# Optimization experiments

Measured on AMD Instinct MI355X. Metric: run time of the kernel, lower is better.

Reference implementation:

```python
import jax, jax.numpy as jnp
import numpy as np

B, T, C, H = 8, 2048, 1024, 64

def setup_inputs() -> dict:
    key = jax.random.key(0)
    k1, k2, k3, k4 = jax.random.split(key, 4)
    x = jax.random.normal(k1, (B, T, C), dtype=jnp.float32)
    sw = 1.0 / np.sqrt(C)  # Linear-like init scale
    Wq = jax.random.normal(k2, (C, H), dtype=jnp.float32) * sw
    Wk = jax.random.normal(k3, (C, H), dtype=jnp.float32) * sw
    Wv = jax.random.normal(k4, (C, H), dtype=jnp.float32) * sw
    return {"x": x, "Wq": Wq, "Wk": Wk, "Wv": Wv}

def reference(x, Wq, Wk, Wv):
    # Single-head causal self-attention (eval mode: dropout is identity).
    # Quantized GEMMs (QLinear / qmatmul) are represented by exact fp32 math.
    Bx, Tx, Cx = x.shape
    q = jnp.einsum('btc,ch->bth', x, Wq)          # [B,T,H]
    k = jnp.einsum('btc,ch->bth', x, Wk)          # [B,T,H]
    v = jnp.einsum('btc,ch->bth', x, Wv)          # [B,T,H]
    scale = k.shape[-1] ** -0.5
    wei = jnp.einsum('bth,bsh->bts', q, k) * scale  # [B,T,T]
    causal = jnp.tril(jnp.ones((Tx, Tx), dtype=bool))
    wei = jnp.where(causal, wei, -jnp.inf)
    wei = jax.nn.softmax(wei, axis=-1)
    out = jnp.einsum('bts,bsh->bth', wei, v)      # [B,T,H]
    return out
```

## Files before the change

kernel.cpp:

```cpp
#include <hip/hip_runtime.h>
#include <math.h>

#define Bz 8
#define Tz 2048
#define Cz 1024
#define Hz 64
#define BT (Bz*Tz)

typedef __attribute__((ext_vector_type(8))) short bf16x8;
typedef __attribute__((ext_vector_type(4))) float f32x4;
typedef __attribute__((ext_vector_type(4))) unsigned short us4;

#define PSTRIDE 4160

__device__ __forceinline__ unsigned short f2bf(float f) {
    union { float f; unsigned u; } v; v.f = f;
    unsigned r = v.u + 0x7fffu + ((v.u >> 16) & 1u);
    return (unsigned short)(r >> 16);
}

__device__ __forceinline__ bf16x8 pack8(const float* s) {
    bf16x8 r;
#pragma unroll
    for (int j = 0; j < 8; j++) r[j] = (short)f2bf(s[j]);
    return r;
}

__device__ __forceinline__ unsigned cvt_pk_bf16(float lo, float hi) {
    unsigned r;
    asm volatile("v_cvt_pk_bf16_f32 %0, %1, %2" : "=v"(r) : "v"(lo), "v"(hi));
    return r;
}

__device__ __forceinline__ bf16x8 cvt8(float4 a, float4 b) {
    union { unsigned u[4]; bf16x8 v; } r;
    r.u[0] = cvt_pk_bf16(a.x, a.y);
    r.u[1] = cvt_pk_bf16(a.z, a.w);
    r.u[2] = cvt_pk_bf16(b.x, b.y);
    r.u[3] = cvt_pk_bf16(b.z, b.w);
    return r.v;
}

__device__ __forceinline__ void gload16(const void* g, void* l) {
    __builtin_amdgcn_global_load_lds(
        (const __attribute__((address_space(1))) void*)g,
        (__attribute__((address_space(3))) void*)l, 16, 0, 0);
}

__global__ __launch_bounds__(256)
void wprep_kernel(const float* __restrict__ Wq, const float* __restrict__ Wk,
                  const float* __restrict__ Wv, unsigned short* __restrict__ Wti)
{
    __shared__ float T[64][65];
    const int mat = blockIdx.x >> 4;
    const int kt  = blockIdx.x & 15;
    const int k0  = kt * 64;
    const float* W = (mat == 0) ? Wq : (mat == 1) ? Wk : Wv;
    const int t  = threadIdx.x;
    const int rr = t >> 2;
    const int c4 = (t & 3) * 16;
#pragma unroll
    for (int j = 0; j < 4; j++) {
        float4 w4 = *(const float4*)&W[(size_t)(k0 + rr) * Hz + c4 + j * 4];
        T[c4 + j*4 + 0][rr] = w4.x;
        T[c4 + j*4 + 1][rr] = w4.y;
        T[c4 + j*4 + 2][rr] = w4.z;
        T[c4 + j*4 + 3][rr] = w4.w;
    }
    __syncthreads();
    const int nn  = t >> 2;
    const int sl0 = (t & 3) * 2;
    const int n   = mat * 64 + nn;
    float tmp[16];
#pragma unroll
    for (int j = 0; j < 16; j++) tmp[j] = T[nn][sl0 * 8 + j];
    unsigned short* base = &Wti[(size_t)kt * 12288 + n * 64];
    *(bf16x8*)&base[((sl0    ) ^ (n & 7)) * 8] = pack8(tmp);
    *(bf16x8*)&base[((sl0 + 1) ^ (n & 7)) * 8] = pack8(tmp + 8);
}

__global__ __launch_bounds__(256, 4)
void qkv_mfma_kernel(const float* __restrict__ x, const unsigned short* __restrict__ Wti,
                     unsigned short* __restrict__ qg, unsigned short* __restrict__ kg,
                     unsigned short* __restrict__ vT)
{
    __shared__ __align__(16) float          xsF[2][64 * 64];
    __shared__ __align__(16) unsigned short ws [2][96 * 64];

    const int t    = threadIdx.x;
    const int bid  = blockIdx.x;
    const int u    = bid >> 3;
    const int cb   = u & 1;
    const int M0   = (((u >> 1) * 8) + (bid & 7)) * 64;
    const int ln   = t & 15;
    const int g    = (t & 63) >> 4;
    const int g4   = g * 4;
    const int w    = t >> 6;
    const int lane = t & 63;
    const float SCq = 0.18033688011112042f;

    f32x4 acc[6];
#pragma unroll
    for (int i = 0; i < 6; i++) acc[i] = (f32x4){0.f, 0.f, 0.f, 0.f};

    auto issue = [&](int buf, int kt) {
        const int k0 = kt * 64;
#pragma unroll
        for (int j = 0; j < 4; j++) {
            const int r  = w * 16 + j * 4 + (lane >> 4);
            const int sl = (lane & 15) ^ (r & 7);
            gload16(&x[(size_t)(M0 + r) * Cz + k0 + sl * 4],
                    &xsF[buf][(w * 16 + j * 4) * 64]);
        }
#pragma unroll
        for (int j = 0; j < 3; j++) {
            const int jj = w * 3 + j;
            gload16(&Wti[(size_t)kt * 12288 + (size_t)(cb * 96 + jj * 8) * 64 + lane * 8],
                    &ws[buf][jj * 512]);
        }
    };

    issue(0, 0); issue(1, 1);
    asm volatile("s_waitcnt vmcnt(7)" ::: "memory");
    __builtin_amdgcn_sched_barrier(0);
    __builtin_amdgcn_s_barrier();

    for (int kt = 0; kt < 16; ++kt) {
        const int bufR = kt & 1;
        bf16x8 af[2];
        const int row = w * 16 + ln;
#pragma unroll
        for (int kc = 0; kc < 2; kc++) {
            const int s0 = kc * 8 + g * 2;
            float4 fa = *(const float4*)&xsF[bufR][row * 64 + ((s0    ) ^ (row & 7)) * 4];
            float4 fb = *(const float4*)&xsF[bufR][row * 64 + ((s0 + 1) ^ (row & 7)) * 4];
            af[kc] = cvt8(fa, fb);
        }
        __builtin_amdgcn_s_setprio(1);
#pragma unroll
        for (int ct = 0; ct < 6; ct++) {
            const int nn = ct * 16 + ln;
#pragma unroll
            for (int kc = 0; kc < 2; kc++) {
                bf16x8 bf = *(const bf16x8*)&ws[bufR][nn * 64 + ((kc*4 + g) ^ (nn & 7)) * 8];
                acc[ct] = __builtin_amdgcn_mfma_f32_16x16x32_bf16(af[kc], bf, acc[ct], 0, 0, 0);
            }
        }
        __builtin_amdgcn_s_setprio(0);

        if (kt == 15) break;

        __builtin_amdgcn_sched_barrier(0);
        __builtin_amdgcn_s_barrier();

        if (kt + 2 < 16) {
            issue(bufR, kt + 2);
            asm volatile("s_waitcnt vmcnt(7)" ::: "memory");
        } else {
            asm volatile("s_waitcnt vmcnt(0)" ::: "memory");
        }
        __builtin_amdgcn_sched_barrier(0);
        __builtin_amdgcn_s_barrier();
    }

#pragma unroll
    for (int ct = 0; ct < 6; ct++) {
        const int col0 = cb * 96 + ct * 16;
        const int mat  = col0 >> 6;
        const int cl   = (col0 & 63) + ln;
        const int m0   = M0 + w * 16 + g4;
        if (mat == 0) {
#pragma unroll
            for (int i = 0; i < 4; i++)
                qg[(size_t)(m0 + i) * Hz + cl] = f2bf(acc[ct][i] * SCq);
        } else if (mat == 1) {
#pragma unroll
            for (int i = 0; i < 4; i++)
                kg[(size_t)(m0 + i) * Hz + cl] = f2bf(acc[ct][i]);
        } else {
            const int b = m0 >> 11, tt = m0 & 2047;
            us4 pk;
#pragma unroll
            for (int i = 0; i < 4; i++) pk[i] = f2bf(acc[ct][i]);
            *(us4*)&vT[((size_t)b * Hz + cl) * Tz + tt] = pk;
        }
    }
}

template<int S>
__global__ __launch_bounds__(256, 4)
void attn_mfma_kernel(const unsigned short* __restrict__ qg,
                      const unsigned short* __restrict__ kg,
                      const unsigned short* __restrict__ vT,
                      float* __restrict__ pbase)
{
    __shared__ __align__(16) unsigned short Ks [2][64 * 64];
    __shared__ __align__(16) unsigned short Vts[2][64 * 64];
    __shared__ __align__(16) unsigned short Ps [4 * 16 * 64];

    const int bid = blockIdx.x;
    const int b   = bid & 7;
    const int r0  = bid >> 3;
    const int c   = r0 % S;
    const int qt  = 31 - (r0 / S);
    if (c > qt) return;
    const int q0  = qt * 64;

    const int t  = threadIdx.x;
    const int ln = t & 15;
    const int g  = (t & 63) >> 4;
    const int g4 = g * 4;
    const int w  = t >> 6;
    const int l6 = t & 63;

    const unsigned short* qb = qg + (size_t)b * Tz * Hz;
    const unsigned short* kb = kg + (size_t)b * Tz * Hz;
    const unsigned short* vb = vT + (size_t)b * Hz * Tz;

    const int rl  = l6 >> 3;
    const int swz = ((l6 & 7) ^ rl) * 8;
    auto issue_tile = [&](int buf, int s0) {
#pragma unroll
        for (int qq = 0; qq < 2; qq++) {
            const int row = w*16 + qq*8 + rl;
            gload16(&kb[(size_t)(s0 + row) * Hz + swz],
                    &Ks[buf][(w*16 + qq*8) * 64]);
            gload16(&vb[(size_t)row * Tz + s0 + swz],
                    &Vts[buf][(w*16 + qq*8) * 64]);
        }
    };

    issue_tile(0, c * 64);

    bf16x8 qf[2];
    {
        const int qrow = q0 + w*16 + ln;
        qf[0] = *(const bf16x8*)&qb[(size_t)qrow * Hz + g*8];
        qf[1] = *(const bf16x8*)&qb[(size_t)qrow * Hz + 32 + g*8];
    }

    f32x4 accO[4];
#pragma unroll
    for (int i = 0; i < 4; i++) accO[i] = (f32x4){0.f, 0.f, 0.f, 0.f};
    float lrow = 0.f;
    unsigned short* Pw = &Ps[w * 1024];
    const int pwbase = ln*64 + (g & 1) * 4;
    const int pslotx = (g >> 1);

    __syncthreads();
    int cur = 0;

    for (int s = c; s <= qt; s += S) {
        if (s + S <= qt) issue_tile(cur ^ 1, (s + S) * 64);

        const unsigned short* Kc = &Ks[cur][0];
        const unsigned short* Vc = &Vts[cur][0];

        f32x4 accS[4];
        __builtin_amdgcn_s_setprio(1);
#pragma unroll
        for (int t4 = 0; t4 < 4; t4++) {
            accS[t4] = (f32x4){0.f, 0.f, 0.f, 0.f};
#pragma unroll
            for (int kc = 0; kc < 2; kc++) {
                const int n = t4*16 + ln;
                bf16x8 kf = *(const bf16x8*)&Kc[n*64 + ((kc*4 + g) ^ (n & 7)) * 8];
                accS[t4] = __builtin_amdgcn_mfma_f32_16x16x32_bf16(kf, qf[kc], accS[t4], 0, 0, 0);
            }
        }
        __builtin_amdgcn_s_setprio(0);

        const bool diag = (s == qt);
#pragma unroll
        for (int t4 = 0; t4 < 4; t4++) {
            float pv[4];
#pragma unroll
            for (int i = 0; i < 4; i++) {
                float sv = accS[t4][i];
                if (diag && (t4*16 + g4 + i > w*16 + ln)) sv = -1e30f;
                const float p = exp2f(sv);
                lrow += p;
                pv[i] = p;
            }
            uint2 pk2;
            pk2.x = cvt_pk_bf16(pv[0], pv[1]);
            pk2.y = cvt_pk_bf16(pv[2], pv[3]);
            *(uint2*)&Pw[pwbase + ((t4*2 + pslotx) ^ (ln & 7)) * 8] = pk2;
        }

        __builtin_amdgcn_s_setprio(1);
#pragma unroll
        for (int kc = 0; kc < 2; kc++) {
            bf16x8 pa = *(const bf16x8*)&Pw[ln*64 + ((kc*4 + g) ^ (ln & 7)) * 8];
#pragma unroll
            for (int ht = 0; ht < 4; ht++) {
                const int vr2 = ht*16 + ln;
                bf16x8 vf = *(const bf16x8*)&Vc[vr2*64 + ((kc*4 + g) ^ (vr2 & 7)) * 8];
                accO[ht] = __builtin_amdgcn_mfma_f32_16x16x32_bf16(pa, vf, accO[ht], 0, 0, 0);
            }
        }
        __builtin_amdgcn_s_setprio(0);

        __syncthreads();
        cur ^= 1;
    }

    lrow += __shfl_xor(lrow, 16);
    lrow += __shfl_xor(lrow, 32);

    float* Op = pbase + (size_t)((b * 32 + qt) * S + c) * PSTRIDE;
#pragma unroll
    for (int ht = 0; ht < 4; ht++)
#pragma unroll
        for (int i = 0; i < 4; i++)
            Op[(size_t)(w*16 + g4 + i) * 64 + ht*16 + ln] = accO[ht][i];
    if (g == 0)
        Op[4096 + w*16 + ln] = lrow;
}

template<int S>
__global__ __launch_bounds__(256)
void combine_kernel(const float* __restrict__ pbase, float* __restrict__ out)
{
    const int bid = blockIdx.x;
    const int b   = bid & 7;
    const int qt  = 31 - (bid >> 3);
    const int t   = threadIdx.x;
    const int r   = t >> 2;
    const int cg  = t & 3;

    const int nch = (qt + 1 < S) ? (qt + 1) : S;
    const float* P0 = pbase + (size_t)(b * 32 + qt) * S * PSTRIDE;

    float denom = 0.f;
    float4 o[4];
#pragma unroll
    for (int j = 0; j < 4; j++) o[j] = make_float4(0.f, 0.f, 0.f, 0.f);
    for (int cc = 0; cc < nch; cc++) {
        const float* Pc = P0 + (size_t)cc * PSTRIDE;
        denom += Pc[4096 + r];
#pragma unroll
        for (int j = 0; j < 4; j++) {
            float4 v4 = *(const float4*)&Pc[(size_t)r * 64 + cg * 16 + j * 4];
            o[j].x += v4.x; o[j].y += v4.y; o[j].z += v4.z; o[j].w += v4.w;
        }
    }
    const float inv = 1.f / denom;
    float* ob = out + ((size_t)b * Tz + qt * 64 + r) * Hz + cg * 16;
#pragma unroll
    for (int j = 0; j < 4; j++)
        *(float4*)&ob[j * 4] = make_float4(o[j].x * inv, o[j].y * inv,
                                           o[j].z * inv, o[j].w * inv);
}

extern "C" void kernel_launch(void* const* d_in, const int* in_sizes, int n_in,
                              void* d_out, int out_size, void* d_ws, size_t ws_size,
                              hipStream_t stream) {
    const float* x  = (const float*)d_in[0];
    const float* Wq = (const float*)d_in[1];
    const float* Wk = (const float*)d_in[2];
    const float* Wv = (const float*)d_in[3];

    unsigned short* Wti = (unsigned short*)d_ws;
    unsigned short* qg  = Wti + 196608;
    unsigned short* kg  = qg + (size_t)BT * Hz;
    unsigned short* vT  = kg + (size_t)BT * Hz;
    const size_t baseShorts = 196608 + 3 * (size_t)BT * Hz;
    float* pbase = (float*)((char*)d_ws + baseShorts * 2);
    float* out = (float*)d_out;

    wprep_kernel<<<48, 256, 0, stream>>>(Wq, Wk, Wv, Wti);
    qkv_mfma_kernel<<<512, 256, 0, stream>>>(x, Wti, qg, kg, vT);

    const size_t base = baseShorts * 2;
    const size_t per  = (size_t)8 * 32 * PSTRIDE * 4;
    if (ws_size >= base + 4 * per) {
        attn_mfma_kernel<4><<<8 * 32 * 4, 256, 0, stream>>>(qg, kg, vT, pbase);
        combine_kernel<4><<<256, 256, 0, stream>>>(pbase, out);
    } else {
        attn_mfma_kernel<1><<<8 * 32 * 1, 256, 0, stream>>>(qg, kg, vT, pbase);
        combine_kernel<1><<<256, 256, 0, stream>>>(pbase, out);
    }
}
```

Measured before the change: 47.88 us.

## Process two query tiles per attention block and store partials in bf16

Each attention block now handles 128 query rows (two 64-row halves) and shares each loaded K/V tile between both halves. This halves K/V global and LDS traffic per query and the number of blocks. Split-K partial outputs are written as bf16 instead of fp32, which cuts partial-buffer traffic for the combine kernel at some precision cost. The block count drops to 512 and per-thread register use rises, which may lower occupancy.

Result: slower. 51.85 us (+8.3%).

```diff
diff --git a/kernel.cpp b/kernel.cpp
--- a/kernel.cpp
+++ b/kernel.cpp
@@ -11,7 +11,7 @@
 typedef __attribute__((ext_vector_type(4))) float f32x4;
 typedef __attribute__((ext_vector_type(4))) unsigned short us4;
 
-#define PSTRIDE 4160
+#define PBYTES 16896
 
 __device__ __forceinline__ unsigned short f2bf(float f) {
     union { float f; unsigned u; } v; v.f = f;
@@ -152,7 +152,6 @@
 
         __builtin_amdgcn_sched_barrier(0);
         __builtin_amdgcn_s_barrier();
-
         if (kt + 2 < 16) {
             issue(bufR, kt + 2);
             asm volatile("s_waitcnt vmcnt(7)" ::: "memory");
@@ -192,7 +191,7 @@
 void attn_mfma_kernel(const unsigned short* __restrict__ qg,
                       const unsigned short* __restrict__ kg,
                       const unsigned short* __restrict__ vT,
-                      float* __restrict__ pbase)
+                      char* __restrict__ pbase)
 {
     __shared__ __align__(16) unsigned short Ks [2][64 * 64];
     __shared__ __align__(16) unsigned short Vts[2][64 * 64];
@@ -200,11 +199,12 @@
 
     const int bid = blockIdx.x;
     const int b   = bid & 7;
-    const int r0  = bid >> 3;
-    const int c   = r0 % S;
-    const int qt  = 31 - (r0 / S);
-    if (c > qt) return;
-    const int q0  = qt * 64;
+    const int idx = bid >> 3;
+    const int c   = idx % S;
+    const int qt2 = 15 - (idx / S);
+    const int smax = 2 * qt2 + 1;
+    if (c > smax) return;
+    const int q0  = qt2 * 128;
 
     const int t  = threadIdx.x;
     const int ln = t & 15;
@@ -232,17 +232,23 @@
 
     issue_tile(0, c * 64);
 
-    bf16x8 qf[2];
+    bf16x8 qf0[2], qf1[2];
     {
-        const int qrow = q0 + w*16 + ln;
-        qf[0] = *(const bf16x8*)&qb[(size_t)qrow * Hz + g*8];
-        qf[1] = *(const bf16x8*)&qb[(size_t)qrow * Hz + 32 + g*8];
-    }
-
-    f32x4 accO[4];
-#pragma unroll
-    for (int i = 0; i < 4; i++) accO[i] = (f32x4){0.f, 0.f, 0.f, 0.f};
-    float lrow = 0.f;
+        const int qr0 = q0 + w*16 + ln;
+        qf0[0] = *(const bf16x8*)&qb[(size_t)qr0 * Hz + g*8];
+        qf0[1] = *(const bf16x8*)&qb[(size_t)qr0 * Hz + 32 + g*8];
+        const int qr1 = q0 + 64 + w*16 + ln;
+        qf1[0] = *(const bf16x8*)&qb[(size_t)qr1 * Hz + g*8];
+        qf1[1] = *(const bf16x8*)&qb[(size_t)qr1 * Hz + 32 + g*8];
+    }
+
+    f32x4 accO0[4], accO1[4];
+#pragma unroll
+    for (int i = 0; i < 4; i++) {
+        accO0[i] = (f32x4){0.f, 0.f, 0.f, 0.f};
+        accO1[i] = (f32x4){0.f, 0.f, 0.f, 0.f};
+    }
+    float lrow0 = 0.f, lrow1 = 0.f;
     unsigned short* Pw = &Ps[w * 1024];
     const int pwbase = ln*64 + (g & 1) * 4;
     const int pslotx = (g >> 1);
@@ -250,107 +256,123 @@
     __syncthreads();
     int cur = 0;
 
-    for (int s = c; s <= qt; s += S) {
-        if (s + S <= qt) issue_tile(cur ^ 1, (s + S) * 64);
+#define DO_HALF(QF, ACCO, LROW, DIAG)                                          \
+    {                                                                          \
+        f32x4 accS[4];                                                         \
+        __builtin_amdgcn_s_setprio(1);                                         \
+        _Pragma("unroll")                                                      \
+        for (int t4 = 0; t4 < 4; t4++) {                                       \
+            accS[t4] = (f32x4){0.f, 0.f, 0.f, 0.f};                            \
+            _Pragma("unroll")                                                  \
+            for (int kc = 0; kc < 2; kc++) {                                   \
+                const int n = t4*16 + ln;                                      \
+                bf16x8 kf = *(const bf16x8*)&Kc[n*64 + ((kc*4 + g) ^ (n & 7)) * 8]; \
+                accS[t4] = __builtin_amdgcn_mfma_f32_16x16x32_bf16(kf, QF[kc], accS[t4], 0, 0, 0); \
+            }                                                                  \
+        }                                                                      \
+        __builtin_amdgcn_s_setprio(0);                                         \
+        _Pragma("unroll")                                                      \
+        for (int t4 = 0; t4 < 4; t4++) {                                       \
+            float pv[4];                                                       \
+            _Pragma("unroll")                                                  \
+            for (int i = 0; i < 4; i++) {                                      \
+                float sv = accS[t4][i];                                        \
+                if ((DIAG) && (t4*16 + g4 + i > w*16 + ln)) sv = -1e30f;       \
+                const float p = exp2f(sv);                                     \
+                LROW += p;                                                     \
+                pv[i] = p;                                                     \
+            }                                                                  \
+            uint2 pk2;                                                         \
+            pk2.x = cvt_pk_bf16(pv[0], pv[1]);                                 \
+            pk2.y = cvt_pk_bf16(pv[2], pv[3]);                                 \
+            *(uint2*)&Pw[pwbase + ((t4*2 + pslotx) ^ (ln & 7)) * 8] = pk2;     \
+        }                                                                      \
+        __builtin_amdgcn_s_setprio(1);                                         \
+        _Pragma("unroll")                                                      \
+        for (int kc = 0; kc < 2; kc++) {                                       \
+            bf16x8 pa = *(const bf16x8*)&Pw[ln*64 + ((kc*4 + g) ^ (ln & 7)) * 8]; \
+            _Pragma("unroll")                                                  \
+            for (int ht = 0; ht < 4; ht++) {                                   \
+                const int vr2 = ht*16 + ln;                                    \
+                bf16x8 vf = *(const bf16x8*)&Vc[vr2*64 + ((kc*4 + g) ^ (vr2 & 7)) * 8]; \
+                ACCO[ht] = __builtin_amdgcn_mfma_f32_16x16x32_bf16(pa, vf, ACCO[ht], 0, 0, 0); \
+            }                                                                  \
+        }                                                                      \
+        __builtin_amdgcn_s_setprio(0);                                         \
+    }
+
+    for (int s = c; s <= smax; s += S) {
+        if (s + S <= smax) issue_tile(cur ^ 1, (s + S) * 64);
 
         const unsigned short* Kc = &Ks[cur][0];
         const unsigned short* Vc = &Vts[cur][0];
 
-        f32x4 accS[4];
-        __builtin_amdgcn_s_setprio(1);
-#pragma unroll
-        for (int t4 = 0; t4 < 4; t4++) {
-            accS[t4] = (f32x4){0.f, 0.f, 0.f, 0.f};
-#pragma unroll
-            for (int kc = 0; kc < 2; kc++) {
-                const int n = t4*16 + ln;
-                bf16x8 kf = *(const bf16x8*)&Kc[n*64 + ((kc*4 + g) ^ (n & 7)) * 8];
-                accS[t4] = __builtin_amdgcn_mfma_f32_16x16x32_bf16(kf, qf[kc], accS[t4], 0, 0, 0);
-            }
-        }
-        __builtin_amdgcn_s_setprio(0);
-
-        const bool diag = (s == qt);
-#pragma unroll
-        for (int t4 = 0; t4 < 4; t4++) {
-            float pv[4];
-#pragma unroll
-            for (int i = 0; i < 4; i++) {
-                float sv = accS[t4][i];
-                if (diag && (t4*16 + g4 + i > w*16 + ln)) sv = -1e30f;
-                const float p = exp2f(sv);
-                lrow += p;
-                pv[i] = p;
-            }
-            uint2 pk2;
-            pk2.x = cvt_pk_bf16(pv[0], pv[1]);
-            pk2.y = cvt_pk_bf16(pv[2], pv[3]);
-            *(uint2*)&Pw[pwbase + ((t4*2 + pslotx) ^ (ln & 7)) * 8] = pk2;
-        }
-
-        __builtin_amdgcn_s_setprio(1);
-#pragma unroll
-        for (int kc = 0; kc < 2; kc++) {
-            bf16x8 pa = *(const bf16x8*)&Pw[ln*64 + ((kc*4 + g) ^ (ln & 7)) * 8];
-#pragma unroll
-            for (int ht = 0; ht < 4; ht++) {
-                const int vr2 = ht*16 + ln;
-                bf16x8 vf = *(const bf16x8*)&Vc[vr2*64 + ((kc*4 + g) ^ (vr2 & 7)) * 8];
-                accO[ht] = __builtin_amdgcn_mfma_f32_16x16x32_bf16(pa, vf, accO[ht], 0, 0, 0);
-            }
-        }
-        __builtin_amdgcn_s_setprio(0);
+        if (s != smax) DO_HALF(qf0, accO0, lrow0, (s == smax - 1));
+        DO_HALF(qf1, accO1, lrow1, (s == smax));
 
         __syncthreads();
         cur ^= 1;
     }
-
-    lrow += __shfl_xor(lrow, 16);
-    lrow += __shfl_xor(lrow, 32);
-
-    float* Op = pbase + (size_t)((b * 32 + qt) * S + c) * PSTRIDE;
+#undef DO_HALF
+
+    lrow0 += __shfl_xor(lrow0, 16); lrow0 += __shfl_xor(lrow0, 32);
+    lrow1 += __shfl_xor(lrow1, 16); lrow1 += __shfl_xor(lrow1, 32);
+
+    char* Op = pbase + (size_t)((b * 16 + qt2) * S + c) * PBYTES;
+    unsigned short* Ob = (unsigned short*)Op;
+    float* Lp = (float*)(Op + 16384);
 #pragma unroll
     for (int ht = 0; ht < 4; ht++)
 #pragma unroll
-        for (int i = 0; i < 4; i++)
-            Op[(size_t)(w*16 + g4 + i) * 64 + ht*16 + ln] = accO[ht][i];
-    if (g == 0)
-        Op[4096 + w*16 + ln] = lrow;
+        for (int i = 0; i < 4; i++) {
+            Ob[(size_t)(w*16 + g4 + i) * 64 + ht*16 + ln]        = f2bf(accO0[ht][i]);
+            Ob[(size_t)(64 + w*16 + g4 + i) * 64 + ht*16 + ln]   = f2bf(accO1[ht][i]);
+        }
+    if (g == 0) {
+        Lp[w*16 + ln]      = lrow0;
+        Lp[64 + w*16 + ln] = lrow1;
+    }
 }
 
 template<int S>
 __global__ __launch_bounds__(256)
-void combine_kernel(const float* __restrict__ pbase, float* __restrict__ out)
+void combine_kernel(const char* __restrict__ pbase, float* __restrict__ out)
 {
     const int bid = blockIdx.x;
     const int b   = bid & 7;
-    const int qt  = 31 - (bid >> 3);
+    const int qt2 = bid >> 3;
     const int t   = threadIdx.x;
-    const int r   = t >> 2;
-    const int cg  = t & 3;
-
-    const int nch = (qt + 1 < S) ? (qt + 1) : S;
-    const float* P0 = pbase + (size_t)(b * 32 + qt) * S * PSTRIDE;
+    const int r   = t >> 1;
+    const int cg  = (t & 1) * 32;
+
+    const int nch = (2*qt2 + 2 < S) ? (2*qt2 + 2) : S;
+    const char* P0 = pbase + (size_t)((b * 16 + qt2) * S) * PBYTES;
 
     float denom = 0.f;
-    float4 o[4];
-#pragma unroll
-    for (int j = 0; j < 4; j++) o[j] = make_float4(0.f, 0.f, 0.f, 0.f);
+    float o[32];
+#pragma unroll
+    for (int j = 0; j < 32; j++) o[j] = 0.f;
     for (int cc = 0; cc < nch; cc++) {
-        const float* Pc = P0 + (size_t)cc * PSTRIDE;
-        denom += Pc[4096 + r];
-#pragma unroll
-        for (int j = 0; j < 4; j++) {
-            float4 v4 = *(const float4*)&Pc[(size_t)r * 64 + cg * 16 + j * 4];
-            o[j].x += v4.x; o[j].y += v4.y; o[j].z += v4.z; o[j].w += v4.w;
+        const char* Pc = P0 + (size_t)cc * PBYTES;
+        const unsigned short* Ob = (const unsigned short*)Pc;
+        denom += ((const float*)(Pc + 16384))[r];
+#pragma unroll
+        for (int j = 0; j < 8; j++) {
+            us4 v = *(const us4*)&Ob[(size_t)r * 64 + cg + j * 4];
+#pragma unroll
+            for (int e = 0; e < 4; e++) {
+                union { unsigned u; float f; } cv;
+                cv.u = ((unsigned)v[e]) << 16;
+                o[j*4 + e] += cv.f;
+            }
         }
     }
     const float inv = 1.f / denom;
-    float* ob = out + ((size_t)b * Tz + qt * 64 + r) * Hz + cg * 16;
-#pragma unroll
-    for (int j = 0; j < 4; j++)
-        *(float4*)&ob[j * 4] = make_float4(o[j].x * inv, o[j].y * inv,
-                                           o[j].z * inv, o[j].w * inv);
+    float* ob = out + ((size_t)b * Tz + qt2 * 128 + r) * Hz + cg;
+#pragma unroll
+    for (int j = 0; j < 8; j++)
+        *(float4*)&ob[j * 4] = make_float4(o[j*4] * inv, o[j*4+1] * inv,
+                                           o[j*4+2] * inv, o[j*4+3] * inv);
 }
 
 extern "C" void kernel_launch(void* const* d_in, const int* in_sizes, int n_in,
@@ -366,19 +388,19 @@
     unsigned short* kg  = qg + (size_t)BT * Hz;
     unsigned short* vT  = kg + (size_t)BT * Hz;
     const size_t baseShorts = 196608 + 3 * (size_t)BT * Hz;
-    float* pbase = (float*)((char*)d_ws + baseShorts * 2);
+    char* pbase = (char*)d_ws + baseShorts * 2;
     float* out = (float*)d_out;
 
     wprep_kernel<<<48, 256, 0, stream>>>(Wq, Wk, Wv, Wti);
     qkv_mfma_kernel<<<512, 256, 0, stream>>>(x, Wti, qg, kg, vT);
 
     const size_t base = baseShorts * 2;
-    const size_t per  = (size_t)8 * 32 * PSTRIDE * 4;
+    const size_t per  = (size_t)8 * 16 * PBYTES;
     if (ws_size >= base + 4 * per) {
-        attn_mfma_kernel<4><<<8 * 32 * 4, 256, 0, stream>>>(qg, kg, vT, pbase);
-        combine_kernel<4><<<256, 256, 0, stream>>>(pbase, out);
+        attn_mfma_kernel<4><<<16 * 4 * 8, 256, 0, stream>>>(qg, kg, vT, pbase);
+        combine_kernel<4><<<128, 256, 0, stream>>>(pbase, out);
     } else {
-        attn_mfma_kernel<1><<<8 * 32 * 1, 256, 0, stream>>>(qg, kg, vT, pbase);
-        combine_kernel<1><<<256, 256, 0, stream>>>(pbase, out);
-    }
-}
+        attn_mfma_kernel<1><<<16 * 1 * 8, 256, 0, stream>>>(qg, kg, vT, pbase);
+        combine_kernel<1><<<128, 256, 0, stream>>>(pbase, out);
+    }
+}
```
